# Optimization experiments

Measured on AMD Instinct MI355X. Metric: run time of the kernel, lower is better.

## Reference

```python
import jax, jax.numpy as jnp
import numpy as np

S, H, HEADS = 2048, 1024, 16   # seq_len, hidden_size, num attention heads
E, NM, P = 256, 1024, 2048     # num entities, total mentions, num candidate pairs
PH = 1024                      # pair_hidden_size


def setup_inputs() -> dict:
    key = jax.random.key(0)
    ks = jax.random.split(key, 13)
    s = 1.0 / np.sqrt(H)
    return {
        "sequence_output": jax.random.normal(ks[0], (S, H), jnp.float32),
        "attention": jax.random.uniform(ks[1], (HEADS, S, S), jnp.float32),
        "mention_idx": jax.random.randint(ks[2], (NM,), 0, S, jnp.int32),
        "entity_ids": jnp.sort(jax.random.randint(ks[3], (NM,), 0, E, jnp.int32)),
        "pair_h": jax.random.randint(ks[4], (P,), 0, E, jnp.int32),
        "pair_t": jax.random.randint(ks[5], (P,), 0, E, jnp.int32),
        "W_head": jax.random.normal(ks[6], (H, PH), jnp.float32) * s,
        "b_head": jnp.zeros((PH,), jnp.float32),
        "W_tail": jax.random.normal(ks[7], (H, PH), jnp.float32) * s,
        "b_tail": jnp.zeros((PH,), jnp.float32),
        "W_ctx": jax.random.normal(ks[8], (H, PH), jnp.float32) * s,
        "W_bil": jax.random.normal(ks[9], (PH, PH), jnp.float32) * s,
        "b_bil": jnp.zeros((), jnp.float32),
    }


def reference(sequence_output, attention, mention_idx, entity_ids, pair_h, pair_t,
              W_head, b_head, W_tail, b_tail, W_ctx, W_bil, b_bil):
    # ---- entity aggregation: ragged segment logsumexp (embs) + segment mean (atts) ----
    vals = sequence_output[mention_idx]                               # [NM, H]
    counts = jax.ops.segment_sum(jnp.ones((NM,), vals.dtype), entity_ids, num_segments=E)
    has = counts > 0                                                  # [E]
    seg_max = jax.ops.segment_max(vals, entity_ids, num_segments=E)   # [E, H]
    seg_max = jnp.where(has[:, None], seg_max, 0.0)
    sums = jax.ops.segment_sum(jnp.exp(vals - seg_max[entity_ids]), entity_ids, num_segments=E)
    ent_emb = jnp.where(has[:, None],
                        seg_max + jnp.log(jnp.where(has[:, None], sums, 1.0)),
                        0.0)                                          # [E, H]
    m_att = jnp.transpose(attention[:, mention_idx, :], (1, 0, 2))    # [NM, HEADS, S]
    ent_att = jax.ops.segment_sum(m_att, entity_ids, num_segments=E)
    ent_att = ent_att / jnp.maximum(counts, 1.0)[:, None, None]       # [E, HEADS, S]

    # ---- pair scoring ----
    hs, ts = ent_emb[pair_h], ent_emb[pair_t]                         # [P, H]
    pair_att = (ent_att[pair_h] * ent_att[pair_t]).sum(axis=1)        # [P, S]
    pair_att = pair_att / (pair_att.sum(axis=-1, keepdims=True) + 1e-6)
    contexts = pair_att @ sequence_output                             # [P, H]
    ctx_p = contexts @ W_ctx                                          # [P, PH]
    z_s = jnp.tanh(hs @ W_head + b_head + ctx_p)
    z_o = jnp.tanh(ts @ W_tail + b_tail + ctx_p)
    logits = jnp.einsum('pi,ij,pj->p', z_s, W_bil, z_o) + b_bil       # [P]
    return logits
```

## Files before the change

kernel.cpp:

```cpp
#include <hip/hip_runtime.h>
#include <hip/hip_bf16.h>
#include <math.h>
#include <stdint.h>

#define S_LEN  2048
#define HID    1024
#define NHEADS 16
#define NE     256
#define NMEN   1024
#define NP     2048
#define PHID   1024

typedef __attribute__((ext_vector_type(8))) short bf16x8;
typedef __attribute__((ext_vector_type(4))) float f32x4;
typedef unsigned int uint;

__device__ inline void seg_bounds(const int* __restrict__ entity_ids, int e,
                                  int& start, int& end) {
    int lo = 0, hi = NMEN;
    while (lo < hi) { int mid = (lo + hi) >> 1; if (entity_ids[mid] < e) lo = mid + 1; else hi = mid; }
    start = lo;
    hi = NMEN;
    while (lo < hi) { int mid = (lo + hi) >> 1; if (entity_ids[mid] <= e) lo = mid + 1; else hi = mid; }
    end = lo;
}

__device__ __forceinline__ void load_lds16(const void* g, void* l) {
    __builtin_amdgcn_global_load_lds(
        (const __attribute__((address_space(1))) uint32_t*)g,
        (__attribute__((address_space(3))) uint32_t*)l,
        16, 0, 0);
}

__device__ __forceinline__ float bflo(uint u) { return __uint_as_float(u << 16); }
__device__ __forceinline__ float bfhi(uint u) { return __uint_as_float(u & 0xffff0000u); }
__device__ __forceinline__ uint pk2(float a, float b) {
    __hip_bfloat16 ha = __float2bfloat16(a), hb = __float2bfloat16(b);
    unsigned short ua = *(unsigned short*)&ha, ub = *(unsigned short*)&hb;
    return (uint)ua | ((uint)ub << 16);
}

__global__ void prep_ent_kernel(const float* __restrict__ seq,
                                const float* __restrict__ attention,
                                const float* __restrict__ w0, const float* __restrict__ w1,
                                const float* __restrict__ w2, const float* __restrict__ wbil,
                                const int* __restrict__ mention_idx,
                                const int* __restrict__ entity_ids,
                                __hip_bfloat16* __restrict__ seqB,
                                __hip_bfloat16* __restrict__ o0, __hip_bfloat16* __restrict__ o1,
                                __hip_bfloat16* __restrict__ o2, __hip_bfloat16* __restrict__ obil,
                                uint2* __restrict__ eaB,
                                __hip_bfloat16* __restrict__ ent_emb)
{
    __shared__ float tbuf[32][33];
    __shared__ int sb[2];
    int id = blockIdx.x;
    if (id < 1024) {
        long i = (long)id * 256 + threadIdx.x;
        const float4* in4 = (const float4*)seq;
        float4 a = in4[2 * i], b = in4[2 * i + 1];
        uint4 o;
        o.x = pk2(a.x, a.y); o.y = pk2(a.z, a.w);
        o.z = pk2(b.x, b.y); o.w = pk2(b.z, b.w);
        ((uint4*)seqB)[i] = o;
        return;
    }
    if (id < 4096) {
        int t = id - 1024;
        int z = t >> 10;
        const float* in = (z == 0) ? w0 : (z == 1) ? w1 : w2;
        __hip_bfloat16* out = (z == 0) ? o0 : (z == 1) ? o1 : o2;
        int r0 = ((t >> 5) & 31) * 32, c0 = (t & 31) * 32;
        int j = threadIdx.x & 31, i0 = threadIdx.x >> 5;
        for (int i = i0; i < 32; i += 8)
            tbuf[i][j] = in[(long)(r0 + i) * 1024 + c0 + j];
        __syncthreads();
        for (int i = i0; i < 32; i += 8)
            out[(long)(c0 + i) * 1024 + r0 + j] = __float2bfloat16(tbuf[j][i]);
        return;
    }
    if (id < 4608) {
        long i = (long)(id - 4096) * 256 + threadIdx.x;
        const float4* in4 = (const float4*)wbil;
        float4 a = in4[2 * i], b = in4[2 * i + 1];
        uint4 o;
        o.x = pk2(a.x, a.y); o.y = pk2(a.z, a.w);
        o.z = pk2(b.x, b.y); o.w = pk2(b.z, b.w);
        ((uint4*)obil)[i] = o;
        return;
    }
    int t = id - 4608;
    int e = t & 255, role = t >> 8;
    if (threadIdx.x == 0) { int s, tt; seg_bounds(entity_ids, e, s, tt); sb[0] = s; sb[1] = tt; }
    __syncthreads();
    int start = sb[0], end = sb[1];

    if (role < 16) {
        const float4* att4 = (const float4*)attention;
        int h = role;
        float inv = 1.f / fmaxf((float)(end - start), 1.f);
        for (int s4 = threadIdx.x; s4 < S_LEN / 4; s4 += 256) {
            float ax = 0.f, ay = 0.f, az = 0.f, aw = 0.f;
            for (int i = start; i < end; ++i) {
                float4 v = att4[((long)h * S_LEN + mention_idx[i]) * (S_LEN / 4) + s4];
                ax += v.x; ay += v.y; az += v.z; aw += v.w;
            }
            uint2 o; o.x = pk2(ax * inv, ay * inv); o.y = pk2(az * inv, aw * inv);
            eaB[((long)e * NHEADS + h) * (S_LEN / 4) + s4] = o;
        }
    } else {
        const float4* seq4 = (const float4*)seq;
        int col4 = threadIdx.x;
        uint2 o;
        if (end <= start) {
            o.x = 0; o.y = 0;
            ((uint2*)ent_emb)[(long)e * 256 + col4] = o;
            return;
        }
        float mx = -INFINITY, my = -INFINITY, mz = -INFINITY, mw = -INFINITY;
        for (int i = start; i < end; ++i) {
            float4 v = seq4[(long)mention_idx[i] * 256 + col4];
            mx = fmaxf(mx, v.x); my = fmaxf(my, v.y); mz = fmaxf(mz, v.z); mw = fmaxf(mw, v.w);
        }
        float sx = 0.f, sy = 0.f, sz = 0.f, sw = 0.f;
        for (int i = start; i < end; ++i) {
            float4 v = seq4[(long)mention_idx[i] * 256 + col4];
            sx += expf(v.x - mx); sy += expf(v.y - my); sz += expf(v.z - mz); sw += expf(v.w - mw);
        }
        o.x = pk2(mx + logf(sx), my + logf(sy));
        o.y = pk2(mz + logf(sz), mw + logf(sw));
        ((uint2*)ent_emb)[(long)e * 256 + col4] = o;
    }
}

template <int MODE>
__device__ __forceinline__ void gemm_core(
    const __hip_bfloat16* __restrict__ A,
    const __hip_bfloat16* __restrict__ Bt,
    void* __restrict__ Cout, const __hip_bfloat16* __restrict__ zvec, float* __restrict__ out,
    int M, int N, int Kstride, int kLen,
    int bx, int by, int bz,
    short (*As)[128][8], short (*Bs)[128][8])
{
    int tid = threadIdx.x;
    int lane = tid & 63, wid = tid >> 6;
    int wr = wid >> 1, wc = wid & 1;
    int bm = by * 128, bn = bx * 128;
    int kBeg = bz * kLen;

    const __hip_bfloat16* gsrc[8];
    void* ldst[8];
#pragma unroll
    for (int i = 0; i < 8; ++i) {
        int c = wid * 8 + i;
        int isA = (c < 16) ? 1 : 0;
        int cc = isA ? c : c - 16;
        int kg2 = cc >> 1, rh = cc & 1;
        gsrc[i] = (isA ? A + (long)(bm + rh * 64 + lane) * Kstride
                       : Bt + (long)(bn + rh * 64 + lane) * Kstride) + kBeg + kg2 * 8;
        ldst[i] = isA ? (void*)&As[kg2][rh * 64][0] : (void*)&Bs[kg2][rh * 64][0];
    }

    f32x4 acc[4][4] = {};
    int kg = lane >> 4, lr = lane & 15;

    for (int k0 = 0; k0 < kLen; k0 += 64) {
#pragma unroll
        for (int i = 0; i < 8; ++i)
            load_lds16(gsrc[i] + k0, ldst[i]);
        __syncthreads();
#pragma unroll
        for (int sub = 0; sub < 2; ++sub) {
            bf16x8 af[4], bfr[4];
#pragma unroll
            for (int f = 0; f < 4; ++f) {
                af[f]  = *(const bf16x8*)&As[sub * 4 + kg][wr * 64 + f * 16 + lr][0];
                bfr[f] = *(const bf16x8*)&Bs[sub * 4 + kg][wc * 64 + f * 16 + lr][0];
            }
#pragma unroll
            for (int fm = 0; fm < 4; ++fm)
#pragma unroll
                for (int fn = 0; fn < 4; ++fn)
                    acc[fm][fn] = __builtin_amdgcn_mfma_f32_16x16x32_bf16(af[fm], bfr[fn], acc[fm][fn], 0, 0, 0);
        }
        __syncthreads();
    }

    int q4 = (lane >> 4) * 4;
    if (MODE == 0) {
#pragma unroll
        for (int fm = 0; fm < 4; ++fm)
#pragma unroll
            for (int fn = 0; fn < 4; ++fn) {
                int row = bm + wr * 64 + fm * 16 + q4;
                int col = bn + wc * 64 + fn * 16 + lr;
#pragma unroll
                for (int r = 0; r < 4; ++r)
                    ((float*)Cout)[((long)bz * M + row + r) * N + col] = acc[fm][fn][r];
            }
    } else if (MODE == 1) {
#pragma unroll
        for (int fm = 0; fm < 4; ++fm)
#pragma unroll
            for (int fn = 0; fn < 4; ++fn) {
                int row = bm + wr * 64 + fm * 16 + q4;
                int col = bn + wc * 64 + fn * 16 + lr;
#pragma unroll
                for (int r = 0; r < 4; ++r)
                    ((__hip_bfloat16*)Cout)[(long)(row + r) * N + col] = __float2bfloat16(acc[fm][fn][r]);
            }
    } else if (MODE == 3) {
#pragma unroll
        for (int fm = 0; fm < 4; ++fm)
#pragma unroll
            for (int fn = 0; fn < 4; ++fn) {
                int row = bm + wr * 64 + fm * 16 + q4;
                int col = bn + wc * 64 + fn * 16 + lr;
#pragma unroll
                for (int r = 0; r < 4; ++r)
                    ((__hip_bfloat16*)Cout)[((long)bz * M + row + r) * N + col] = __float2bfloat16(acc[fm][fn][r]);
            }
    } else {
#pragma unroll
        for (int fm = 0; fm < 4; ++fm) {
#pragma unroll
            for (int r = 0; r < 4; ++r) {
                int row = bm + wr * 64 + fm * 16 + q4 + r;
                float v = 0.f;
#pragma unroll
                for (int fn = 0; fn < 4; ++fn) {
                    int col = bn + wc * 64 + fn * 16 + lr;
                    v += acc[fm][fn][r] * __bfloat162float(zvec[(long)row * N + col]);
                }
                v += __shfl_xor(v, 1, 64);
                v += __shfl_xor(v, 2, 64);
                v += __shfl_xor(v, 4, 64);
                v += __shfl_xor(v, 8, 64);
                if (lr == 0) atomicAdd(out + row, v);
            }
        }
    }
}

__launch_bounds__(256)
__global__ void pair_seqw_ehet(const __hip_bfloat16* __restrict__ WctxT,
                               const __hip_bfloat16* __restrict__ seqB,
                               __hip_bfloat16* __restrict__ seqWT,
                               const __hip_bfloat16* __restrict__ embB,
                               const __hip_bfloat16* __restrict__ WhtT,
                               float* __restrict__ ehetP,
                               const uint4* __restrict__ ea,
                               const int* __restrict__ pair_h,
                               const int* __restrict__ pair_t,
                               uint4* __restrict__ patt)
{
    __shared__ short As[8][128][8];
    __shared__ short Bs[8][128][8];
    int id = blockIdx.x;
    if (id < 128) {
        gemm_core<1>(WctxT, seqB, seqWT, nullptr, nullptr,
                     PHID, S_LEN, HID, HID, id & 15, id >> 4, 0, As, Bs);
        return;
    }
    if (id < 256) {
        int u = id - 128;
        gemm_core<0>(embB, WhtT, ehetP, nullptr, nullptr,
                     NE, 2 * PHID, HID, HID / 4, u & 15, (u >> 4) & 1, u >> 5, As, Bs);
        return;
    }
    __shared__ float wsum[4];
    int p = id - 256;
    long bh = (long)pair_h[p] * NHEADS * (S_LEN / 8);
    long bt = (long)pair_t[p] * NHEADS * (S_LEN / 8);
    int s8 = threadIdx.x;
    float a0 = 0, a1 = 0, a2 = 0, a3 = 0, a4 = 0, a5 = 0, a6 = 0, a7 = 0;
#pragma unroll
    for (int h = 0; h < NHEADS; ++h) {
        uint4 xa = ea[bh + h * (S_LEN / 8) + s8];
        uint4 xb = ea[bt + h * (S_LEN / 8) + s8];
        a0 += bflo(xa.x) * bflo(xb.x); a1 += bfhi(xa.x) * bfhi(xb.x);
        a2 += bflo(xa.y) * bflo(xb.y); a3 += bfhi(xa.y) * bfhi(xb.y);
        a4 += bflo(xa.z) * bflo(xb.z); a5 += bfhi(xa.z) * bfhi(xb.z);
        a6 += bflo(xa.w) * bflo(xb.w); a7 += bfhi(xa.w) * bfhi(xb.w);
    }
    float psum = a0 + a1 + a2 + a3 + a4 + a5 + a6 + a7;
#pragma unroll
    for (int off = 32; off > 0; off >>= 1)
        psum += __shfl_down(psum, off, 64);
    int lane = threadIdx.x & 63, wid = threadIdx.x >> 6;
    if (lane == 0) wsum[wid] = psum;
    __syncthreads();
    float inv = 1.f / (wsum[0] + wsum[1] + wsum[2] + wsum[3] + 1e-6f);
    uint4 o;
    o.x = pk2(a0 * inv, a1 * inv); o.y = pk2(a2 * inv, a3 * inv);
    o.z = pk2(a4 * inv, a5 * inv); o.w = pk2(a6 * inv, a7 * inv);
    patt[(long)p * (S_LEN / 8) + s8] = o;
}

__launch_bounds__(256)
__global__ void gemm_ctxp_reduce(const __hip_bfloat16* __restrict__ pattB,
                                 const __hip_bfloat16* __restrict__ seqWT,
                                 __hip_bfloat16* __restrict__ ctxpB,
                                 const float* __restrict__ ehetP,
                                 float* __restrict__ ehet)
{
    __shared__ short As[8][128][8];
    __shared__ short Bs[8][128][8];
    int id = blockIdx.x;
    if (id < 512) {
        int f = (id & 7) * 64 + (id >> 3);
        int bx = f >> 6, inner = f & 63;
        int by = inner & 15, bz = inner >> 4;
        gemm_core<3>(pattB, seqWT, ctxpB, nullptr, nullptr,
                     NP, PHID, S_LEN, S_LEN / 4, bx, by, bz, As, Bs);
        return;
    }
    long i = (long)(id - 512) * 2048 + (long)threadIdx.x * 8;
    const long n = (long)NE * 2 * PHID;
    float4 s0 = make_float4(0.f, 0.f, 0.f, 0.f), s1 = s0;
#pragma unroll
    for (int s = 0; s < 4; ++s) {
        float4 a = *(const float4*)&ehetP[s * n + i];
        float4 b = *(const float4*)&ehetP[s * n + i + 4];
        s0.x += a.x; s0.y += a.y; s0.z += a.z; s0.w += a.w;
        s1.x += b.x; s1.y += b.y; s1.z += b.z; s1.w += b.w;
    }
    *(float4*)&ehet[i] = s0;
    *(float4*)&ehet[i + 4] = s1;
}

__global__ void zs_zo_kernel(const __hip_bfloat16* __restrict__ ctxpB,
                             const float* __restrict__ ehet,
                             const float* __restrict__ b_head,
                             const float* __restrict__ b_tail,
                             const int* __restrict__ pair_h,
                             const int* __restrict__ pair_t,
                             __hip_bfloat16* __restrict__ zs,
                             __hip_bfloat16* __restrict__ zo,
                             const float* __restrict__ b_bil, float* __restrict__ out)
{
    long base = ((long)blockIdx.x * 256 + threadIdx.x) * 4;
    if (base < NP) {
        float bb = b_bil[0];
#pragma unroll
        for (int i = 0; i < 4; ++i) out[base + i] = bb;
    }
    int p = (int)(base >> 10);
    int j = (int)(base & (PHID - 1));
    const long n = (long)NP * PHID;
    float c0 = 0.f, c1 = 0.f, c2 = 0.f, c3 = 0.f;
#pragma unroll
    for (int s = 0; s < 4; ++s) {
        uint2 u = *(const uint2*)&ctxpB[s * n + base];
        c0 += bflo(u.x); c1 += bfhi(u.x); c2 += bflo(u.y); c3 += bfhi(u.y);
    }
    float4 eh = *(const float4*)&ehet[(long)pair_h[p] * 2048 + j];
    float4 et = *(const float4*)&ehet[(long)pair_t[p] * 2048 + 1024 + j];
    float4 bh = *(const float4*)&b_head[j];
    float4 bt = *(const float4*)&b_tail[j];
    float h0 = tanhf(eh.x + bh.x + c0), h1 = tanhf(eh.y + bh.y + c1);
    float h2 = tanhf(eh.z + bh.z + c2), h3 = tanhf(eh.w + bh.w + c3);
    float t0 = tanhf(et.x + bt.x + c0), t1 = tanhf(et.y + bt.y + c1);
    float t2 = tanhf(et.z + bt.z + c2), t3 = tanhf(et.w + bt.w + c3);
    uint2 ozs; ozs.x = pk2(h0, h1); ozs.y = pk2(h2, h3);
    uint2 ozo; ozo.x = pk2(t0, t1); ozo.y = pk2(t2, t3);
    *(uint2*)&zs[base] = ozs;
    *(uint2*)&zo[base] = ozo;
}

template <int MODE>
__launch_bounds__(256)
__global__ void gemm_single(const __hip_bfloat16* __restrict__ A,
                            const __hip_bfloat16* __restrict__ Bt,
                            void* __restrict__ Cout,
                            const __hip_bfloat16* __restrict__ zvec,
                            float* __restrict__ out,
                            int M, int N, int Kstride, int kLen)
{
    __shared__ short As[8][128][8];
    __shared__ short Bs[8][128][8];
    gemm_core<MODE>(A, Bt, Cout, zvec, out, M, N, Kstride, kLen,
                    blockIdx.x, blockIdx.y, blockIdx.z, As, Bs);
}

extern "C" void kernel_launch(void* const* d_in, const int* in_sizes, int n_in,
                              void* d_out, int out_size, void* d_ws, size_t ws_size,
                              hipStream_t stream)
{
    const float* seq        = (const float*)d_in[0];
    const float* attention  = (const float*)d_in[1];
    const int*   mention_idx= (const int*)  d_in[2];
    const int*   entity_ids = (const int*)  d_in[3];
    const int*   pair_h     = (const int*)  d_in[4];
    const int*   pair_t     = (const int*)  d_in[5];
    const float* W_head     = (const float*)d_in[6];
    const float* b_head     = (const float*)d_in[7];
    const float* W_tail     = (const float*)d_in[8];
    const float* b_tail     = (const float*)d_in[9];
    const float* W_ctx      = (const float*)d_in[10];
    const float* W_bil      = (const float*)d_in[11];
    const float* b_bil      = (const float*)d_in[12];
    float* out = (float*)d_out;

    char* w = (char*)d_ws;
    __hip_bfloat16* seqB  = (__hip_bfloat16*)(w + 0);
    __hip_bfloat16* WctxT = (__hip_bfloat16*)(w + (4l << 20));
    __hip_bfloat16* WhtT  = (__hip_bfloat16*)(w + (6l << 20));
    __hip_bfloat16* WbilB = (__hip_bfloat16*)(w + (10l << 20));
    __hip_bfloat16* embB  = (__hip_bfloat16*)(w + (12l << 20));
    __hip_bfloat16* eaB   = (__hip_bfloat16*)(w + (13l << 20));
    __hip_bfloat16* pattB = (__hip_bfloat16*)(w + (29l << 20));
    __hip_bfloat16* seqWT = (__hip_bfloat16*)(w + (37l << 20));
    __hip_bfloat16* zsB   = (__hip_bfloat16*)(w + (41l << 20));
    __hip_bfloat16* zoB   = (__hip_bfloat16*)(w + (45l << 20));
    __hip_bfloat16* ctxpB = (__hip_bfloat16*)(w + (49l << 20));
    float* ehetP = (float*)(w + (65l << 20));
    float* ehet  = (float*)(w + (73l << 20));

    prep_ent_kernel<<<8960, 256, 0, stream>>>(seq, attention, W_ctx, W_head, W_tail, W_bil,
                                              mention_idx, entity_ids,
                                              seqB, WctxT, WhtT, WhtT + (long)PHID * HID, WbilB,
                                              (uint2*)eaB, embB);

    pair_seqw_ehet<<<2304, 256, 0, stream>>>(WctxT, seqB, seqWT, embB, WhtT, ehetP,
                                             (const uint4*)eaB, pair_h, pair_t, (uint4*)pattB);

    gemm_ctxp_reduce<<<768, 256, 0, stream>>>(pattB, seqWT, ctxpB, ehetP, ehet);

    zs_zo_kernel<<<2048, 256, 0, stream>>>(ctxpB, ehet, b_head, b_tail, pair_h, pair_t,
                                           zsB, zoB, b_bil, out);

    gemm_single<2><<<dim3(8, 16, 2), 256, 0, stream>>>(zoB, WbilB, nullptr, zsB, out,
                                                       NP, PHID, HID, HID / 2);
}
```

Baseline: 139.8 us.

## Double-buffer LDS in ctxp and bilinear GEMMs and raise bilinear split-K

Adds a double-buffered GEMM core that issues the global-to-LDS loads for the next K-step while MFMAs run on the current buffer, with one barrier per step instead of two. It is used for the ctx_p GEMM and the final bilinear GEMM, and the bilinear GEMM's split-K grows from 2 to 4. The aim is to hide load latency and put more blocks on the device. In exchange LDS per block doubles to 64KB, which can lower occupancy, and there are more atomic adds into the output.

```diff
diff --git a/kernel.cpp b/kernel.cpp
--- a/kernel.cpp
+++ b/kernel.cpp
@@ -134,58 +134,12 @@
 }
 
 template <int MODE>
-__device__ __forceinline__ void gemm_core(
-    const __hip_bfloat16* __restrict__ A,
-    const __hip_bfloat16* __restrict__ Bt,
-    void* __restrict__ Cout, const __hip_bfloat16* __restrict__ zvec, float* __restrict__ out,
-    int M, int N, int Kstride, int kLen,
-    int bx, int by, int bz,
-    short (*As)[128][8], short (*Bs)[128][8])
-{
-    int tid = threadIdx.x;
-    int lane = tid & 63, wid = tid >> 6;
-    int wr = wid >> 1, wc = wid & 1;
-    int bm = by * 128, bn = bx * 128;
-    int kBeg = bz * kLen;
-
-    const __hip_bfloat16* gsrc[8];
-    void* ldst[8];
-#pragma unroll
-    for (int i = 0; i < 8; ++i) {
-        int c = wid * 8 + i;
-        int isA = (c < 16) ? 1 : 0;
-        int cc = isA ? c : c - 16;
-        int kg2 = cc >> 1, rh = cc & 1;
-        gsrc[i] = (isA ? A + (long)(bm + rh * 64 + lane) * Kstride
-                       : Bt + (long)(bn + rh * 64 + lane) * Kstride) + kBeg + kg2 * 8;
-        ldst[i] = isA ? (void*)&As[kg2][rh * 64][0] : (void*)&Bs[kg2][rh * 64][0];
-    }
-
-    f32x4 acc[4][4] = {};
-    int kg = lane >> 4, lr = lane & 15;
-
-    for (int k0 = 0; k0 < kLen; k0 += 64) {
-#pragma unroll
-        for (int i = 0; i < 8; ++i)
-            load_lds16(gsrc[i] + k0, ldst[i]);
-        __syncthreads();
-#pragma unroll
-        for (int sub = 0; sub < 2; ++sub) {
-            bf16x8 af[4], bfr[4];
-#pragma unroll
-            for (int f = 0; f < 4; ++f) {
-                af[f]  = *(const bf16x8*)&As[sub * 4 + kg][wr * 64 + f * 16 + lr][0];
-                bfr[f] = *(const bf16x8*)&Bs[sub * 4 + kg][wc * 64 + f * 16 + lr][0];
-            }
-#pragma unroll
-            for (int fm = 0; fm < 4; ++fm)
-#pragma unroll
-                for (int fn = 0; fn < 4; ++fn)
-                    acc[fm][fn] = __builtin_amdgcn_mfma_f32_16x16x32_bf16(af[fm], bfr[fn], acc[fm][fn], 0, 0, 0);
-        }
-        __syncthreads();
-    }
-
+__device__ __forceinline__ void gemm_epilogue(
+    f32x4 (&acc)[4][4], void* __restrict__ Cout,
+    const __hip_bfloat16* __restrict__ zvec, float* __restrict__ out,
+    int M, int N, int bm, int bn, int bz, int wr, int wc, int lane)
+{
+    int lr = lane & 15;
     int q4 = (lane >> 4) * 4;
     if (MODE == 0) {
 #pragma unroll
@@ -242,6 +196,123 @@
     }
 }
 
+template <int MODE>
+__device__ __forceinline__ void gemm_core(
+    const __hip_bfloat16* __restrict__ A,
+    const __hip_bfloat16* __restrict__ Bt,
+    void* __restrict__ Cout, const __hip_bfloat16* __restrict__ zvec, float* __restrict__ out,
+    int M, int N, int Kstride, int kLen,
+    int bx, int by, int bz,
+    short (*As)[128][8], short (*Bs)[128][8])
+{
+    int tid = threadIdx.x;
+    int lane = tid & 63, wid = tid >> 6;
+    int wr = wid >> 1, wc = wid & 1;
+    int bm = by * 128, bn = bx * 128;
+    int kBeg = bz * kLen;
+
+    const __hip_bfloat16* gsrc[8];
+    void* ldst[8];
+#pragma unroll
+    for (int i = 0; i < 8; ++i) {
+        int c = wid * 8 + i;
+        int isA = (c < 16) ? 1 : 0;
+        int cc = isA ? c : c - 16;
+        int kg2 = cc >> 1, rh = cc & 1;
+        gsrc[i] = (isA ? A + (long)(bm + rh * 64 + lane) * Kstride
+                       : Bt + (long)(bn + rh * 64 + lane) * Kstride) + kBeg + kg2 * 8;
+        ldst[i] = isA ? (void*)&As[kg2][rh * 64][0] : (void*)&Bs[kg2][rh * 64][0];
+    }
+
+    f32x4 acc[4][4] = {};
+    int kg = lane >> 4, lr = lane & 15;
+
+    for (int k0 = 0; k0 < kLen; k0 += 64) {
+#pragma unroll
+        for (int i = 0; i < 8; ++i)
+            load_lds16(gsrc[i] + k0, ldst[i]);
+        __syncthreads();
+#pragma unroll
+        for (int sub = 0; sub < 2; ++sub) {
+            bf16x8 af[4], bfr[4];
+#pragma unroll
+            for (int f = 0; f < 4; ++f) {
+                af[f]  = *(const bf16x8*)&As[sub * 4 + kg][wr * 64 + f * 16 + lr][0];
+                bfr[f] = *(const bf16x8*)&Bs[sub * 4 + kg][wc * 64 + f * 16 + lr][0];
+            }
+#pragma unroll
+            for (int fm = 0; fm < 4; ++fm)
+#pragma unroll
+                for (int fn = 0; fn < 4; ++fn)
+                    acc[fm][fn] = __builtin_amdgcn_mfma_f32_16x16x32_bf16(af[fm], bfr[fn], acc[fm][fn], 0, 0, 0);
+        }
+        __syncthreads();
+    }
+    gemm_epilogue<MODE>(acc, Cout, zvec, out, M, N, bm, bn, bz, wr, wc, lane);
+}
+
+template <int MODE>
+__device__ __forceinline__ void gemm_core_db(
+    const __hip_bfloat16* __restrict__ A,
+    const __hip_bfloat16* __restrict__ Bt,
+    void* __restrict__ Cout, const __hip_bfloat16* __restrict__ zvec, float* __restrict__ out,
+    int M, int N, int Kstride, int kLen,
+    int bx, int by, int bz,
+    short (*As)[8][128][8], short (*Bs)[8][128][8])
+{
+    int tid = threadIdx.x;
+    int lane = tid & 63, wid = tid >> 6;
+    int wr = wid >> 1, wc = wid & 1;
+    int bm = by * 128, bn = bx * 128;
+    int kBeg = bz * kLen;
+
+    const __hip_bfloat16* gsrc[8];
+    void *ld0[8], *ld1[8];
+#pragma unroll
+    for (int i = 0; i < 8; ++i) {
+        int c = wid * 8 + i;
+        int isA = (c < 16) ? 1 : 0;
+        int cc = isA ? c : c - 16;
+        int kg2 = cc >> 1, rh = cc & 1;
+        gsrc[i] = (isA ? A + (long)(bm + rh * 64 + lane) * Kstride
+                       : Bt + (long)(bn + rh * 64 + lane) * Kstride) + kBeg + kg2 * 8;
+        ld0[i] = isA ? (void*)&As[0][kg2][rh * 64][0] : (void*)&Bs[0][kg2][rh * 64][0];
+        ld1[i] = isA ? (void*)&As[1][kg2][rh * 64][0] : (void*)&Bs[1][kg2][rh * 64][0];
+    }
+
+    f32x4 acc[4][4] = {};
+    int kg = lane >> 4, lr = lane & 15;
+    int nSteps = kLen >> 6;
+
+#define STAGE_DB(t, ld) { _Pragma("unroll") \
+    for (int i = 0; i < 8; ++i) load_lds16(gsrc[i] + (t) * 64, ld[i]); }
+#define COMPUTE_DB(AsB, BsB) { _Pragma("unroll") \
+    for (int sub = 0; sub < 2; ++sub) { \
+        bf16x8 af[4], bfr[4]; \
+        _Pragma("unroll") for (int f = 0; f < 4; ++f) { \
+            af[f]  = *(const bf16x8*)&AsB[sub * 4 + kg][wr * 64 + f * 16 + lr][0]; \
+            bfr[f] = *(const bf16x8*)&BsB[sub * 4 + kg][wc * 64 + f * 16 + lr][0]; \
+        } \
+        _Pragma("unroll") for (int fm = 0; fm < 4; ++fm) \
+        _Pragma("unroll") for (int fn = 0; fn < 4; ++fn) \
+            acc[fm][fn] = __builtin_amdgcn_mfma_f32_16x16x32_bf16(af[fm], bfr[fn], acc[fm][fn], 0, 0, 0); \
+    } }
+
+    STAGE_DB(0, ld0);
+    __syncthreads();
+    for (int step = 0; step < nSteps; step += 2) {
+        STAGE_DB(step + 1, ld1);
+        COMPUTE_DB(As[0], Bs[0]);
+        __syncthreads();
+        if (step + 2 < nSteps) STAGE_DB(step + 2, ld0);
+        COMPUTE_DB(As[1], Bs[1]);
+        __syncthreads();
+    }
+#undef STAGE_DB
+#undef COMPUTE_DB
+    gemm_epilogue<MODE>(acc, Cout, zvec, out, M, N, bm, bn, bz, wr, wc, lane);
+}
+
 __launch_bounds__(256)
 __global__ void pair_seqw_ehet(const __hip_bfloat16* __restrict__ WctxT,
                                const __hip_bfloat16* __restrict__ seqB,
@@ -304,15 +375,15 @@
                                  const float* __restrict__ ehetP,
                                  float* __restrict__ ehet)
 {
-    __shared__ short As[8][128][8];
-    __shared__ short Bs[8][128][8];
+    __shared__ short As[2][8][128][8];
+    __shared__ short Bs[2][8][128][8];
     int id = blockIdx.x;
     if (id < 512) {
         int f = (id & 7) * 64 + (id >> 3);
         int bx = f >> 6, inner = f & 63;
         int by = inner & 15, bz = inner >> 4;
-        gemm_core<3>(pattB, seqWT, ctxpB, nullptr, nullptr,
-                     NP, PHID, S_LEN, S_LEN / 4, bx, by, bz, As, Bs);
+        gemm_core_db<3>(pattB, seqWT, ctxpB, nullptr, nullptr,
+                        NP, PHID, S_LEN, S_LEN / 4, bx, by, bz, As, Bs);
         return;
     }
     long i = (long)(id - 512) * 2048 + (long)threadIdx.x * 8;
@@ -370,17 +441,17 @@
 
 template <int MODE>
 __launch_bounds__(256)
-__global__ void gemm_single(const __hip_bfloat16* __restrict__ A,
-                            const __hip_bfloat16* __restrict__ Bt,
-                            void* __restrict__ Cout,
-                            const __hip_bfloat16* __restrict__ zvec,
-                            float* __restrict__ out,
-                            int M, int N, int Kstride, int kLen)
-{
-    __shared__ short As[8][128][8];
-    __shared__ short Bs[8][128][8];
-    gemm_core<MODE>(A, Bt, Cout, zvec, out, M, N, Kstride, kLen,
-                    blockIdx.x, blockIdx.y, blockIdx.z, As, Bs);
+__global__ void gemm_single_db(const __hip_bfloat16* __restrict__ A,
+                               const __hip_bfloat16* __restrict__ Bt,
+                               void* __restrict__ Cout,
+                               const __hip_bfloat16* __restrict__ zvec,
+                               float* __restrict__ out,
+                               int M, int N, int Kstride, int kLen)
+{
+    __shared__ short As[2][8][128][8];
+    __shared__ short Bs[2][8][128][8];
+    gemm_core_db<MODE>(A, Bt, Cout, zvec, out, M, N, Kstride, kLen,
+                       blockIdx.x, blockIdx.y, blockIdx.z, As, Bs);
 }
 
 extern "C" void kernel_launch(void* const* d_in, const int* in_sizes, int n_in,
@@ -430,6 +501,6 @@
     zs_zo_kernel<<<2048, 256, 0, stream>>>(ctxpB, ehet, b_head, b_tail, pair_h, pair_t,
                                            zsB, zoB, b_bil, out);
 
-    gemm_single<2><<<dim3(8, 16, 2), 256, 0, stream>>>(zoB, WbilB, nullptr, zsB, out,
-                                                       NP, PHID, HID, HID / 2);
-}
+    gemm_single_db<2><<<dim3(8, 16, 4), 256, 0, stream>>>(zoB, WbilB, nullptr, zsB, out,
+                                                          NP, PHID, HID, HID / 4);
+}
```

Measured after the change: 136.6 us. 2.3% less time.

## Fuse ctx GEMM with tanh epilogue, drop split-K reductions, double-buffer LDS

Applied to the files above, without the earlier changes.

The context-projection GEMM now runs over the full K dimension and computes the zs/zo tanh activations in its epilogue. This removes the separate split-K partial buffer, the reduction pass and the zs_zo kernel. The entity head/tail GEMM also drops its 4-way split-K, which removes the ehet partial-sum reduction. A double-buffered LDS loop overlaps global-to-LDS loads with MFMA compute in the fused and bilinear GEMMs, and the bilinear split-K goes from 2 to 4. The trade-off is far fewer blocks for the fused GEMM (128 on a 256-CU part) and longer per-block K loops, so occupancy drops in exchange for less memory traffic and fewer launches.

```diff
diff --git a/kernel.cpp b/kernel.cpp
--- a/kernel.cpp
+++ b/kernel.cpp
@@ -134,58 +134,12 @@
 }
 
 template <int MODE>
-__device__ __forceinline__ void gemm_core(
-    const __hip_bfloat16* __restrict__ A,
-    const __hip_bfloat16* __restrict__ Bt,
-    void* __restrict__ Cout, const __hip_bfloat16* __restrict__ zvec, float* __restrict__ out,
-    int M, int N, int Kstride, int kLen,
-    int bx, int by, int bz,
-    short (*As)[128][8], short (*Bs)[128][8])
-{
-    int tid = threadIdx.x;
-    int lane = tid & 63, wid = tid >> 6;
-    int wr = wid >> 1, wc = wid & 1;
-    int bm = by * 128, bn = bx * 128;
-    int kBeg = bz * kLen;
-
-    const __hip_bfloat16* gsrc[8];
-    void* ldst[8];
-#pragma unroll
-    for (int i = 0; i < 8; ++i) {
-        int c = wid * 8 + i;
-        int isA = (c < 16) ? 1 : 0;
-        int cc = isA ? c : c - 16;
-        int kg2 = cc >> 1, rh = cc & 1;
-        gsrc[i] = (isA ? A + (long)(bm + rh * 64 + lane) * Kstride
-                       : Bt + (long)(bn + rh * 64 + lane) * Kstride) + kBeg + kg2 * 8;
-        ldst[i] = isA ? (void*)&As[kg2][rh * 64][0] : (void*)&Bs[kg2][rh * 64][0];
-    }
-
-    f32x4 acc[4][4] = {};
-    int kg = lane >> 4, lr = lane & 15;
-
-    for (int k0 = 0; k0 < kLen; k0 += 64) {
-#pragma unroll
-        for (int i = 0; i < 8; ++i)
-            load_lds16(gsrc[i] + k0, ldst[i]);
-        __syncthreads();
-#pragma unroll
-        for (int sub = 0; sub < 2; ++sub) {
-            bf16x8 af[4], bfr[4];
-#pragma unroll
-            for (int f = 0; f < 4; ++f) {
-                af[f]  = *(const bf16x8*)&As[sub * 4 + kg][wr * 64 + f * 16 + lr][0];
-                bfr[f] = *(const bf16x8*)&Bs[sub * 4 + kg][wc * 64 + f * 16 + lr][0];
-            }
-#pragma unroll
-            for (int fm = 0; fm < 4; ++fm)
-#pragma unroll
-                for (int fn = 0; fn < 4; ++fn)
-                    acc[fm][fn] = __builtin_amdgcn_mfma_f32_16x16x32_bf16(af[fm], bfr[fn], acc[fm][fn], 0, 0, 0);
-        }
-        __syncthreads();
-    }
-
+__device__ __forceinline__ void gemm_epilogue(
+    f32x4 (&acc)[4][4], void* __restrict__ Cout,
+    const __hip_bfloat16* __restrict__ zvec, float* __restrict__ out,
+    int M, int N, int bm, int bn, int bz, int wr, int wc, int lane)
+{
+    int lr = lane & 15;
     int q4 = (lane >> 4) * 4;
     if (MODE == 0) {
 #pragma unroll
@@ -208,17 +162,6 @@
 #pragma unroll
                 for (int r = 0; r < 4; ++r)
                     ((__hip_bfloat16*)Cout)[(long)(row + r) * N + col] = __float2bfloat16(acc[fm][fn][r]);
-            }
-    } else if (MODE == 3) {
-#pragma unroll
-        for (int fm = 0; fm < 4; ++fm)
-#pragma unroll
-            for (int fn = 0; fn < 4; ++fn) {
-                int row = bm + wr * 64 + fm * 16 + q4;
-                int col = bn + wc * 64 + fn * 16 + lr;
-#pragma unroll
-                for (int r = 0; r < 4; ++r)
-                    ((__hip_bfloat16*)Cout)[((long)bz * M + row + r) * N + col] = __float2bfloat16(acc[fm][fn][r]);
             }
     } else {
 #pragma unroll
@@ -242,13 +185,98 @@
     }
 }
 
+#define COMPUTE_TILE(AsB, BsB) { _Pragma("unroll") \
+    for (int sub = 0; sub < 2; ++sub) { \
+        bf16x8 af[4], bfr[4]; \
+        _Pragma("unroll") for (int f = 0; f < 4; ++f) { \
+            af[f]  = *(const bf16x8*)&AsB[sub * 4 + kg][wr * 64 + f * 16 + lr][0]; \
+            bfr[f] = *(const bf16x8*)&BsB[sub * 4 + kg][wc * 64 + f * 16 + lr][0]; \
+        } \
+        _Pragma("unroll") for (int fm = 0; fm < 4; ++fm) \
+        _Pragma("unroll") for (int fn = 0; fn < 4; ++fn) \
+            acc[fm][fn] = __builtin_amdgcn_mfma_f32_16x16x32_bf16(af[fm], bfr[fn], acc[fm][fn], 0, 0, 0); \
+    } }
+
+template <int MODE>
+__device__ __forceinline__ void gemm_core(
+    const __hip_bfloat16* __restrict__ A,
+    const __hip_bfloat16* __restrict__ Bt,
+    void* __restrict__ Cout, const __hip_bfloat16* __restrict__ zvec, float* __restrict__ out,
+    int M, int N, int Kstride, int kLen,
+    int bx, int by, int bz,
+    short (*As)[128][8], short (*Bs)[128][8])
+{
+    int tid = threadIdx.x;
+    int lane = tid & 63, wid = tid >> 6;
+    int wr = wid >> 1, wc = wid & 1;
+    int bm = by * 128, bn = bx * 128;
+    int kBeg = bz * kLen;
+
+    const __hip_bfloat16* gsrc[8];
+    void* ldst[8];
+#pragma unroll
+    for (int i = 0; i < 8; ++i) {
+        int c = wid * 8 + i;
+        int isA = (c < 16) ? 1 : 0;
+        int cc = isA ? c : c - 16;
+        int kg2 = cc >> 1, rh = cc & 1;
+        gsrc[i] = (isA ? A + (long)(bm + rh * 64 + lane) * Kstride
+                       : Bt + (long)(bn + rh * 64 + lane) * Kstride) + kBeg + kg2 * 8;
+        ldst[i] = isA ? (void*)&As[kg2][rh * 64][0] : (void*)&Bs[kg2][rh * 64][0];
+    }
+
+    f32x4 acc[4][4] = {};
+    int kg = lane >> 4, lr = lane & 15;
+
+    for (int k0 = 0; k0 < kLen; k0 += 64) {
+#pragma unroll
+        for (int i = 0; i < 8; ++i)
+            load_lds16(gsrc[i] + k0, ldst[i]);
+        __syncthreads();
+        COMPUTE_TILE(As, Bs);
+        __syncthreads();
+    }
+    gemm_epilogue<MODE>(acc, Cout, zvec, out, M, N, bm, bn, bz, wr, wc, lane);
+}
+
+#define GEMM_DB_LOOP(A, Bt, Kstride, kLen, bm, bn, kBeg)                       \
+    const __hip_bfloat16* gsrc[8];                                             \
+    void *ld0[8], *ld1[8];                                                     \
+    _Pragma("unroll")                                                          \
+    for (int i = 0; i < 8; ++i) {                                              \
+        int c = wid * 8 + i;                                                   \
+        int isA = (c < 16) ? 1 : 0;                                            \
+        int cc = isA ? c : c - 16;                                             \
+        int kg2 = cc >> 1, rh = cc & 1;                                        \
+        gsrc[i] = (isA ? (A) + (long)((bm) + rh * 64 + lane) * (Kstride)       \
+                       : (Bt) + (long)((bn) + rh * 64 + lane) * (Kstride))     \
+                  + (kBeg) + kg2 * 8;                                          \
+        ld0[i] = isA ? (void*)&As[0][kg2][rh * 64][0] : (void*)&Bs[0][kg2][rh * 64][0]; \
+        ld1[i] = isA ? (void*)&As[1][kg2][rh * 64][0] : (void*)&Bs[1][kg2][rh * 64][0]; \
+    }                                                                          \
+    int nSteps = (kLen) >> 6;                                                  \
+    { _Pragma("unroll") for (int i = 0; i < 8; ++i) load_lds16(gsrc[i], ld0[i]); } \
+    __syncthreads();                                                           \
+    for (int step = 0; step < nSteps; step += 2) {                             \
+        { _Pragma("unroll") for (int i = 0; i < 8; ++i)                        \
+            load_lds16(gsrc[i] + (step + 1) * 64, ld1[i]); }                   \
+        COMPUTE_TILE(As[0], Bs[0]);                                            \
+        __syncthreads();                                                       \
+        if (step + 2 < nSteps) {                                               \
+            _Pragma("unroll") for (int i = 0; i < 8; ++i)                      \
+                load_lds16(gsrc[i] + (step + 2) * 64, ld0[i]);                 \
+        }                                                                      \
+        COMPUTE_TILE(As[1], Bs[1]);                                            \
+        __syncthreads();                                                       \
+    }
+
 __launch_bounds__(256)
 __global__ void pair_seqw_ehet(const __hip_bfloat16* __restrict__ WctxT,
                                const __hip_bfloat16* __restrict__ seqB,
                                __hip_bfloat16* __restrict__ seqWT,
                                const __hip_bfloat16* __restrict__ embB,
                                const __hip_bfloat16* __restrict__ WhtT,
-                               float* __restrict__ ehetP,
+                               float* __restrict__ ehet,
                                const uint4* __restrict__ ea,
                                const int* __restrict__ pair_h,
                                const int* __restrict__ pair_t,
@@ -262,14 +290,14 @@
                      PHID, S_LEN, HID, HID, id & 15, id >> 4, 0, As, Bs);
         return;
     }
-    if (id < 256) {
+    if (id < 160) {
         int u = id - 128;
-        gemm_core<0>(embB, WhtT, ehetP, nullptr, nullptr,
-                     NE, 2 * PHID, HID, HID / 4, u & 15, (u >> 4) & 1, u >> 5, As, Bs);
+        gemm_core<0>(embB, WhtT, ehet, nullptr, nullptr,
+                     NE, 2 * PHID, HID, HID, u & 15, u >> 4, 0, As, Bs);
         return;
     }
     __shared__ float wsum[4];
-    int p = id - 256;
+    int p = id - 160;
     long bh = (long)pair_h[p] * NHEADS * (S_LEN / 8);
     long bt = (long)pair_t[p] * NHEADS * (S_LEN / 8);
     int s8 = threadIdx.x;
@@ -298,89 +326,82 @@
 }
 
 __launch_bounds__(256)
-__global__ void gemm_ctxp_reduce(const __hip_bfloat16* __restrict__ pattB,
-                                 const __hip_bfloat16* __restrict__ seqWT,
-                                 __hip_bfloat16* __restrict__ ctxpB,
-                                 const float* __restrict__ ehetP,
-                                 float* __restrict__ ehet)
-{
-    __shared__ short As[8][128][8];
-    __shared__ short Bs[8][128][8];
+__global__ void gemm_fused_zszo(const __hip_bfloat16* __restrict__ pattB,
+                                const __hip_bfloat16* __restrict__ seqWT,
+                                const float* __restrict__ ehet,
+                                const float* __restrict__ b_head,
+                                const float* __restrict__ b_tail,
+                                const int* __restrict__ pair_h,
+                                const int* __restrict__ pair_t,
+                                __hip_bfloat16* __restrict__ zs,
+                                __hip_bfloat16* __restrict__ zo,
+                                const float* __restrict__ b_bil,
+                                float* __restrict__ out)
+{
+    __shared__ short As[2][8][128][8];
+    __shared__ short Bs[2][8][128][8];
     int id = blockIdx.x;
-    if (id < 512) {
-        int f = (id & 7) * 64 + (id >> 3);
-        int bx = f >> 6, inner = f & 63;
-        int by = inner & 15, bz = inner >> 4;
-        gemm_core<3>(pattB, seqWT, ctxpB, nullptr, nullptr,
-                     NP, PHID, S_LEN, S_LEN / 4, bx, by, bz, As, Bs);
-        return;
-    }
-    long i = (long)(id - 512) * 2048 + (long)threadIdx.x * 8;
-    const long n = (long)NE * 2 * PHID;
-    float4 s0 = make_float4(0.f, 0.f, 0.f, 0.f), s1 = s0;
-#pragma unroll
-    for (int s = 0; s < 4; ++s) {
-        float4 a = *(const float4*)&ehetP[s * n + i];
-        float4 b = *(const float4*)&ehetP[s * n + i + 4];
-        s0.x += a.x; s0.y += a.y; s0.z += a.z; s0.w += a.w;
-        s1.x += b.x; s1.y += b.y; s1.z += b.z; s1.w += b.w;
-    }
-    *(float4*)&ehet[i] = s0;
-    *(float4*)&ehet[i + 4] = s1;
-}
-
-__global__ void zs_zo_kernel(const __hip_bfloat16* __restrict__ ctxpB,
-                             const float* __restrict__ ehet,
-                             const float* __restrict__ b_head,
-                             const float* __restrict__ b_tail,
-                             const int* __restrict__ pair_h,
-                             const int* __restrict__ pair_t,
-                             __hip_bfloat16* __restrict__ zs,
-                             __hip_bfloat16* __restrict__ zo,
-                             const float* __restrict__ b_bil, float* __restrict__ out)
-{
-    long base = ((long)blockIdx.x * 256 + threadIdx.x) * 4;
-    if (base < NP) {
+    int f = (id & 7) * 16 + (id >> 3);
+    int bx = f >> 4, by = f & 15;
+
+    int tid = threadIdx.x;
+    int lane = tid & 63, wid = tid >> 6;
+    int wr = wid >> 1, wc = wid & 1;
+    int bm = by * 128, bn = bx * 128;
+    f32x4 acc[4][4] = {};
+    int kg = lane >> 4, lr = lane & 15;
+
+    GEMM_DB_LOOP(pattB, seqWT, S_LEN, S_LEN, bm, bn, 0)
+
+    int q4 = (lane >> 4) * 4;
+#pragma unroll
+    for (int fn = 0; fn < 4; ++fn) {
+        int col = bn + wc * 64 + fn * 16 + lr;
+        float bh = b_head[col], btl = b_tail[col];
+#pragma unroll
+        for (int fm = 0; fm < 4; ++fm) {
+#pragma unroll
+            for (int r = 0; r < 4; ++r) {
+                int row = bm + wr * 64 + fm * 16 + q4 + r;
+                int ph = pair_h[row], pt = pair_t[row];
+                float c = acc[fm][fn][r];
+                float hv = tanhf(ehet[(long)ph * 2048 + col] + bh + c);
+                float tv = tanhf(ehet[(long)pt * 2048 + 1024 + col] + btl + c);
+                zs[(long)row * PHID + col] = __float2bfloat16(hv);
+                zo[(long)row * PHID + col] = __float2bfloat16(tv);
+            }
+        }
+    }
+    if (bx == 0 && wc == 0 && lr == 0) {
         float bb = b_bil[0];
 #pragma unroll
-        for (int i = 0; i < 4; ++i) out[base + i] = bb;
-    }
-    int p = (int)(base >> 10);
-    int j = (int)(base & (PHID - 1));
-    const long n = (long)NP * PHID;
-    float c0 = 0.f, c1 = 0.f, c2 = 0.f, c3 = 0.f;
-#pragma unroll
-    for (int s = 0; s < 4; ++s) {
-        uint2 u = *(const uint2*)&ctxpB[s * n + base];
-        c0 += bflo(u.x); c1 += bfhi(u.x); c2 += bflo(u.y); c3 += bfhi(u.y);
-    }
-    float4 eh = *(const float4*)&ehet[(long)pair_h[p] * 2048 + j];
-    float4 et = *(const float4*)&ehet[(long)pair_t[p] * 2048 + 1024 + j];
-    float4 bh = *(const float4*)&b_head[j];
-    float4 bt = *(const float4*)&b_tail[j];
-    float h0 = tanhf(eh.x + bh.x + c0), h1 = tanhf(eh.y + bh.y + c1);
-    float h2 = tanhf(eh.z + bh.z + c2), h3 = tanhf(eh.w + bh.w + c3);
-    float t0 = tanhf(et.x + bt.x + c0), t1 = tanhf(et.y + bt.y + c1);
-    float t2 = tanhf(et.z + bt.z + c2), t3 = tanhf(et.w + bt.w + c3);
-    uint2 ozs; ozs.x = pk2(h0, h1); ozs.y = pk2(h2, h3);
-    uint2 ozo; ozo.x = pk2(t0, t1); ozo.y = pk2(t2, t3);
-    *(uint2*)&zs[base] = ozs;
-    *(uint2*)&zo[base] = ozo;
-}
-
-template <int MODE>
+        for (int fm = 0; fm < 4; ++fm)
+#pragma unroll
+            for (int r = 0; r < 4; ++r)
+                out[bm + wr * 64 + fm * 16 + q4 + r] = bb;
+    }
+}
+
 __launch_bounds__(256)
-__global__ void gemm_single(const __hip_bfloat16* __restrict__ A,
-                            const __hip_bfloat16* __restrict__ Bt,
-                            void* __restrict__ Cout,
-                            const __hip_bfloat16* __restrict__ zvec,
-                            float* __restrict__ out,
-                            int M, int N, int Kstride, int kLen)
-{
-    __shared__ short As[8][128][8];
-    __shared__ short Bs[8][128][8];
-    gemm_core<MODE>(A, Bt, Cout, zvec, out, M, N, Kstride, kLen,
-                    blockIdx.x, blockIdx.y, blockIdx.z, As, Bs);
+__global__ void gemm_bilinear_db(const __hip_bfloat16* __restrict__ A,
+                                 const __hip_bfloat16* __restrict__ Bt,
+                                 const __hip_bfloat16* __restrict__ zvec,
+                                 float* __restrict__ out,
+                                 int M, int N, int Kstride, int kLen)
+{
+    __shared__ short As[2][8][128][8];
+    __shared__ short Bs[2][8][128][8];
+    int tid = threadIdx.x;
+    int lane = tid & 63, wid = tid >> 6;
+    int wr = wid >> 1, wc = wid & 1;
+    int bm = blockIdx.y * 128, bn = blockIdx.x * 128;
+    int kBeg = blockIdx.z * kLen;
+    f32x4 acc[4][4] = {};
+    int kg = lane >> 4, lr = lane & 15;
+
+    GEMM_DB_LOOP(A, Bt, Kstride, kLen, bm, bn, kBeg)
+
+    gemm_epilogue<2>(acc, nullptr, zvec, out, M, N, bm, bn, blockIdx.z, wr, wc, lane);
 }
 
 extern "C" void kernel_launch(void* const* d_in, const int* in_sizes, int n_in,
@@ -413,23 +434,19 @@
     __hip_bfloat16* seqWT = (__hip_bfloat16*)(w + (37l << 20));
     __hip_bfloat16* zsB   = (__hip_bfloat16*)(w + (41l << 20));
     __hip_bfloat16* zoB   = (__hip_bfloat16*)(w + (45l << 20));
-    __hip_bfloat16* ctxpB = (__hip_bfloat16*)(w + (49l << 20));
-    float* ehetP = (float*)(w + (65l << 20));
-    float* ehet  = (float*)(w + (73l << 20));
+    float* ehet  = (float*)(w + (49l << 20));
 
     prep_ent_kernel<<<8960, 256, 0, stream>>>(seq, attention, W_ctx, W_head, W_tail, W_bil,
                                               mention_idx, entity_ids,
                                               seqB, WctxT, WhtT, WhtT + (long)PHID * HID, WbilB,
                                               (uint2*)eaB, embB);
 
-    pair_seqw_ehet<<<2304, 256, 0, stream>>>(WctxT, seqB, seqWT, embB, WhtT, ehetP,
+    pair_seqw_ehet<<<2208, 256, 0, stream>>>(WctxT, seqB, seqWT, embB, WhtT, ehet,
                                              (const uint4*)eaB, pair_h, pair_t, (uint4*)pattB);
 
-    gemm_ctxp_reduce<<<768, 256, 0, stream>>>(pattB, seqWT, ctxpB, ehetP, ehet);
-
-    zs_zo_kernel<<<2048, 256, 0, stream>>>(ctxpB, ehet, b_head, b_tail, pair_h, pair_t,
-                                           zsB, zoB, b_bil, out);
-
-    gemm_single<2><<<dim3(8, 16, 2), 256, 0, stream>>>(zoB, WbilB, nullptr, zsB, out,
-                                                       NP, PHID, HID, HID / 2);
-}
+    gemm_fused_zszo<<<128, 256, 0, stream>>>(pattB, seqWT, ehet, b_head, b_tail,
+                                             pair_h, pair_t, zsB, zoB, b_bil, out);
+
+    gemm_bilinear_db<<<dim3(8, 16, 4), 256, 0, stream>>>(zoB, WbilB, zsB, out,
+                                                         NP, PHID, HID, HID / 4);
+}
```

After: 176.7 us. 1.26x slower.
